# Optimization experiments

Measured on AMD Instinct MI355X. Metric: run time of the kernel, lower is better.

## Reference

```python
import jax, jax.numpy as jnp
import numpy as np

N_NODES = 50000
D = 128
N_EDGES = 800000


def _gcn_layer(h, W, b, row, col, mask, n_nodes):
    # Linear: h @ W.T + b  (nn.Linear convention)
    h = h @ W.T + b
    # degree of source nodes, counting only non-self-loop edges (remove_self_loops)
    deg = jax.ops.segment_sum(mask.astype(h.dtype), row, num_segments=n_nodes)
    deg_inv_sqrt = jnp.where(deg > 0, jax.lax.rsqrt(jnp.maximum(deg, 1.0)), 0.0)
    norm = deg_inv_sqrt[row] * deg_inv_sqrt[col] * mask.astype(h.dtype)
    # gather-scale messages [E, D], scatter-add into target nodes (col)
    msg = norm[:, None] * h[row]
    return jax.ops.segment_sum(msg, col, num_segments=n_nodes)


def setup_inputs() -> dict:
    key = jax.random.key(0)
    ks = jax.random.split(key, 9)
    x = jax.random.normal(ks[0], (N_NODES, D), dtype=jnp.float32)
    edge_index = jax.random.randint(ks[1], (2, N_EDGES), 0, N_NODES, dtype=jnp.int64)
    lim = 1.0 / np.sqrt(D)
    params = {}
    for i in range(3):
        params[f"W{i}"] = jax.random.uniform(ks[2 + 2 * i], (D, D), jnp.float32, -lim, lim)
        params[f"b{i}"] = jax.random.uniform(ks[3 + 2 * i], (D,), jnp.float32, -lim, lim)
    return {"x": x, "edge_index": edge_index, **params}


def reference(x, edge_index, W0, b0, W1, b1, W2, b2):
    row, col = edge_index[0], edge_index[1]
    mask = row != col  # remove_self_loops
    h = x
    for W, b in ((W0, b0), (W1, b1), (W2, b2)):
        h_new = jax.nn.relu(_gcn_layer(h, W, b, row, col, mask, x.shape[0]))
        h = h + h_new
    return h
```

## Files before the change

### kernel.cpp

```cpp
#include <hip/hip_runtime.h>
#include <hip/hip_bf16.h>


#define D_DIM 128
#define SCAN_CHUNK 1024
#define CHUNKS 256
#define GROUPS 8
#define GS (CHUNKS / GROUPS)
#define LDSW 12512

typedef __attribute__((ext_vector_type(8))) short bf16x8;
typedef __attribute__((ext_vector_type(4))) float f32x4;

static __device__ __forceinline__ short f2bf(float f) {
    union { __hip_bfloat16 b; short s; } u;
    u.b = __float2bfloat16(f);
    return u.s;
}
static __device__ __forceinline__ float bf_lo(unsigned p) { return __uint_as_float(p << 16); }
static __device__ __forceinline__ float bf_hi(unsigned p) { return __uint_as_float(p & 0xffff0000u); }


__global__ __launch_bounds__(256) void hist_kernel(const int* __restrict__ ei,
                                                   unsigned* __restrict__ partial_col,
                                                   unsigned* __restrict__ partial_row,
                                                   int E, int CHSZ) {
    __shared__ unsigned hh[LDSW];
    int tid = threadIdx.x;
    int ch = blockIdx.x;
    int docol = (blockIdx.y == 0);
    for (int i = tid; i < LDSW; i += 256) hh[i] = 0u;
    __syncthreads();
    int e0 = ch * CHSZ, e1 = min(e0 + CHSZ, E);
    for (int e = e0 + tid; e < e1; e += 256) {
        int row = ei[e];
        int col = ei[E + e];
        if (row == col) continue;
        int bin = docol ? col : row;
        atomicAdd(&hh[bin >> 2], 1u << ((bin & 3) * 8));
    }
    __syncthreads();
    unsigned* dst = (docol ? partial_col : partial_row) + (size_t)ch * LDSW;
    for (int i = tid; i < LDSW; i += 256) dst[i] = hh[i];
}

__global__ __launch_bounds__(256) void group_prefix_kernel(
    unsigned* __restrict__ partial_col, const unsigned* __restrict__ partial_row,
    unsigned* __restrict__ gsum_col, unsigned* __restrict__ gsum_row, int NW) {
    int w = blockIdx.x * 256 + threadIdx.x;
    if (w >= NW) return;
    int g = blockIdx.y;
    size_t base = (size_t)(g * GS) * LDSW + w;
    if (blockIdx.z == 0) {
        unsigned run = 0;
#pragma unroll 4
        for (int c = 0; c < GS; c++) {
            unsigned v = partial_col[base + (size_t)c * LDSW];
            partial_col[base + (size_t)c * LDSW] = run;
            run += v;
        }
        gsum_col[g * NW + w] = run;
    } else {
        unsigned run = 0;
#pragma unroll 4
        for (int c = 0; c < GS; c++) run += partial_row[base + (size_t)c * LDSW];
        gsum_row[g * NW + w] = run;
    }
}

__global__ __launch_bounds__(256) void cnt_dis_kernel(
    const unsigned* __restrict__ gsum_col, const unsigned* __restrict__ gsum_row,
    int* __restrict__ col_cnt, float* __restrict__ dis, int* __restrict__ bsum, int NW) {
    __shared__ int wsum[4];
    int w = blockIdx.x * 256 + threadIdx.x;
    int s = 0;
    if (w < NW) {
        unsigned clo = 0, chi = 0, rlo = 0, rhi = 0;
#pragma unroll
        for (int g = 0; g < GROUPS; g++) {
            unsigned wc = gsum_col[g * NW + w];
            unsigned wr = gsum_row[g * NW + w];
            clo += wc & 0x00FF00FFu; chi += (wc >> 8) & 0x00FF00FFu;
            rlo += wr & 0x00FF00FFu; rhi += (wr >> 8) & 0x00FF00FFu;
        }
        int c0 = clo & 0xFFFF, c1 = chi & 0xFFFF, c2 = clo >> 16, c3 = chi >> 16;
        int r0 = rlo & 0xFFFF, r1 = rhi & 0xFFFF, r2 = rlo >> 16, r3 = rhi >> 16;
        ((int4*)col_cnt)[w] = make_int4(c0, c1, c2, c3);
        float4 dv;
        dv.x = (r0 > 0) ? rsqrtf((float)r0) : 0.0f;
        dv.y = (r1 > 0) ? rsqrtf((float)r1) : 0.0f;
        dv.z = (r2 > 0) ? rsqrtf((float)r2) : 0.0f;
        dv.w = (r3 > 0) ? rsqrtf((float)r3) : 0.0f;
        ((float4*)dis)[w] = dv;
        s = c0 + c1 + c2 + c3;
    }
#pragma unroll
    for (int d = 32; d > 0; d >>= 1) s += __shfl_down(s, d, 64);
    int lane = threadIdx.x & 63, wv = threadIdx.x >> 6;
    if (lane == 0) wsum[wv] = s;
    __syncthreads();
    if (threadIdx.x == 0) bsum[blockIdx.x] = wsum[0] + wsum[1] + wsum[2] + wsum[3];
}

__global__ __launch_bounds__(64) void scan_bbase_kernel(const int* __restrict__ bsum,
                                                        int* __restrict__ bbase,
                                                        int* __restrict__ offs,
                                                        int G, int n) {
    int lane = threadIdx.x;
    int v = (lane < G) ? bsum[lane] : 0;
    int s = v;
#pragma unroll
    for (int d = 1; d < 64; d <<= 1) {
        int t = __shfl_up(s, d, 64);
        if (lane >= d) s += t;
    }
    if (lane < G) bbase[lane] = s - v;
    if (lane == 63) offs[n] = s;
}

__global__ __launch_bounds__(256) void scan_final_kernel(const int* __restrict__ cnt,
                                                         const int* __restrict__ bbase,
                                                         int* __restrict__ offs, int n) {
    __shared__ int wsum[4];
    int base = blockIdx.x * SCAN_CHUNK;
    int tid = threadIdx.x;
    const int PT = SCAN_CHUNK / 256;
    int v[PT];
    int s = 0;
#pragma unroll
    for (int i = 0; i < PT; i++) {
        int g = base + tid * PT + i;
        v[i] = (g < n) ? cnt[g] : 0;
        s += v[i];
    }
    int local_sum = s;
    int lane = tid & 63, w = tid >> 6;
#pragma unroll
    for (int d = 1; d < 64; d <<= 1) {
        int t = __shfl_up(s, d, 64);
        if (lane >= d) s += t;
    }
    if (lane == 63) wsum[w] = s;
    __syncthreads();
    int wbase = 0;
    for (int i = 0; i < w; i++) wbase += wsum[i];
    int run = bbase[blockIdx.x] + wbase + (s - local_sum);
#pragma unroll
    for (int i = 0; i < PT; i++) {
        int g = base + tid * PT + i;
        if (g < n) offs[g] = run;
        run += v[i];
    }
}

__global__ __launch_bounds__(256) void group_base_kernel(
    unsigned* __restrict__ partial_col, const unsigned* __restrict__ gsum_col, int NW) {
    int w = blockIdx.x * 256 + threadIdx.x;
    if (w >= NW) return;
    int g = blockIdx.y + 1;
    unsigned gb = 0;
    for (int gp = 0; gp < g; gp++) gb += gsum_col[gp * NW + w];
    size_t base = (size_t)(g * GS) * LDSW + w;
#pragma unroll 4
    for (int c = 0; c < GS; c++) partial_col[base + (size_t)c * LDSW] += gb;
}

__global__ __launch_bounds__(256) void scatter_kernel(const int* __restrict__ ei,
                                                      const float* __restrict__ dis,
                                                      const int* __restrict__ offs,
                                                      const unsigned* __restrict__ chpref,
                                                      unsigned* __restrict__ epack,
                                                      int E, int CHSZ) {
    __shared__ unsigned cur[LDSW];
    int tid = threadIdx.x;
    int ch = blockIdx.x;
    for (int i = tid; i < LDSW; i += 256) cur[i] = 0u;
    __syncthreads();
    int e0 = ch * CHSZ, e1 = min(e0 + CHSZ, E);
    const unsigned* pf = chpref + (size_t)ch * LDSW;
    for (int e = e0 + tid; e < e1; e += 256) {
        int row = ei[e];
        int col = ei[E + e];
        if (row == col) continue;
        float wgt = dis[row] * dis[col];
        int wd = col >> 2, sh = (col & 3) * 8;
        unsigned old = atomicAdd(&cur[wd], 1u << sh);
        int slot = offs[col] + (int)((pf[wd] >> sh) & 0xFFu) + (int)((old >> sh) & 0xFFu);
        epack[slot] = (unsigned)row | ((unsigned)(unsigned short)f2bf(wgt) << 16);
    }
}

__global__ void wcvt_all_kernel(const float* __restrict__ W0, const float* __restrict__ W1,
                                const float* __restrict__ W2, unsigned short* __restrict__ B0,
                                unsigned short* __restrict__ B1, unsigned short* __restrict__ B2) {
    int i = blockIdx.x * blockDim.x + threadIdx.x;
    const float* W = (blockIdx.y == 0) ? W0 : (blockIdx.y == 1) ? W1 : W2;
    unsigned short* B = (blockIdx.y == 0) ? B0 : (blockIdx.y == 1) ? B1 : B2;
    if (i < D_DIM * D_DIM) B[i] = (unsigned short)f2bf(W[i]);
}


__global__ __launch_bounds__(256) void linear_mfma_kernel(
    const float* __restrict__ A, const unsigned short* __restrict__ Wb,
    const float* __restrict__ bias, unsigned short* __restrict__ hWb, int nrows) {
    __shared__ unsigned short stage[4][16 * 136];
    int wave = threadIdx.x >> 6;
    int lane = threadIdx.x & 63;
    int r0 = blockIdx.x * 64 + wave * 16;
    int m = lane & 15, q = lane >> 4;
    int rload = min(r0 + m, nrows - 1);
    const float4* h4 = (const float4*)A;

    f32x4 acc[8];
#pragma unroll
    for (int jt = 0; jt < 8; jt++) acc[jt] = (f32x4){0.f, 0.f, 0.f, 0.f};

#pragma unroll
    for (int k0 = 0; k0 < 128; k0 += 32) {
        int c0 = k0 + q * 8;
        float4 x0 = h4[rload * 32 + (c0 >> 2)];
        float4 x1 = h4[rload * 32 + (c0 >> 2) + 1];
        bf16x8 a;
        a[0] = f2bf(x0.x); a[1] = f2bf(x0.y); a[2] = f2bf(x0.z); a[3] = f2bf(x0.w);
        a[4] = f2bf(x1.x); a[5] = f2bf(x1.y); a[6] = f2bf(x1.z); a[7] = f2bf(x1.w);
#pragma unroll
        for (int jt = 0; jt < 8; jt++) {
            bf16x8 b = *(const bf16x8*)(Wb + (jt * 16 + m) * D_DIM + c0);
            acc[jt] = __builtin_amdgcn_mfma_f32_16x16x32_bf16(a, b, acc[jt], 0, 0, 0);
        }
    }

#pragma unroll
    for (int jt = 0; jt < 8; jt++) {
        float bv = bias[jt * 16 + m];
#pragma unroll
        for (int reg = 0; reg < 4; reg++)
            stage[wave][(q * 4 + reg) * 136 + jt * 16 + m] =
                (unsigned short)f2bf(acc[jt][reg] + bv);
    }
#pragma unroll
    for (int t = 0; t < 4; t++) {
        int rl = t * 4 + (lane >> 4);
        int gr = r0 + rl;
        if (gr < nrows) {
            uint4 v = *(const uint4*)&stage[wave][rl * 136 + (lane & 15) * 8];
            *(uint4*)&hWb[(size_t)gr * D_DIM + (lane & 15) * 8] = v;
        }
    }
}

__global__ __launch_bounds__(256) void agg_kernel(const int* __restrict__ offs,
                                                  const unsigned* __restrict__ epack,
                                                  const unsigned int* __restrict__ hW2,
                                                  const float* __restrict__ hprev,
                                                  float* __restrict__ hout, int n_nodes) {
    int node = (int)((blockIdx.x * blockDim.x + threadIdx.x) >> 6);
    int lane = threadIdx.x & 63;
    if (node >= n_nodes) return;

    int beg = offs[node];
    int end = offs[node + 1];

    float ax8[8], ay8[8];
#pragma unroll
    for (int u = 0; u < 8; u++) { ax8[u] = 0.f; ay8[u] = 0.f; }

    int i = beg;
    for (; i + 8 <= end; i += 8) {
        unsigned e[8];
        unsigned p[8];
#pragma unroll
        for (int u = 0; u < 8; u++) e[u] = epack[i + u];
#pragma unroll
        for (int u = 0; u < 8; u++) p[u] = hW2[((e[u] & 0xffffu) << 6) + lane];
#pragma unroll
        for (int u = 0; u < 8; u++) {
            float w = bf_hi(e[u]);
            ax8[u] = fmaf(w, bf_lo(p[u]), ax8[u]);
            ay8[u] = fmaf(w, bf_hi(p[u]), ay8[u]);
        }
    }
    int rem = end - i;
    if (rem & 4) {
        unsigned e[4];
        unsigned p[4];
#pragma unroll
        for (int u = 0; u < 4; u++) e[u] = epack[i + u];
#pragma unroll
        for (int u = 0; u < 4; u++) p[u] = hW2[((e[u] & 0xffffu) << 6) + lane];
#pragma unroll
        for (int u = 0; u < 4; u++) {
            float w = bf_hi(e[u]);
            ax8[u] = fmaf(w, bf_lo(p[u]), ax8[u]);
            ay8[u] = fmaf(w, bf_hi(p[u]), ay8[u]);
        }
        i += 4;
    }
    if (rem & 2) {
        unsigned e0 = epack[i], e1 = epack[i + 1];
        unsigned p0 = hW2[((e0 & 0xffffu) << 6) + lane];
        unsigned p1 = hW2[((e1 & 0xffffu) << 6) + lane];
        float w0 = bf_hi(e0), w1 = bf_hi(e1);
        ax8[4] = fmaf(w0, bf_lo(p0), ax8[4]); ay8[4] = fmaf(w0, bf_hi(p0), ay8[4]);
        ax8[5] = fmaf(w1, bf_lo(p1), ax8[5]); ay8[5] = fmaf(w1, bf_hi(p1), ay8[5]);
        i += 2;
    }
    if (rem & 1) {
        unsigned e0 = epack[i];
        unsigned p0 = hW2[((e0 & 0xffffu) << 6) + lane];
        float w0 = bf_hi(e0);
        ax8[6] = fmaf(w0, bf_lo(p0), ax8[6]); ay8[6] = fmaf(w0, bf_hi(p0), ay8[6]);
    }
    float ax = ((ax8[0] + ax8[1]) + (ax8[2] + ax8[3])) + ((ax8[4] + ax8[5]) + (ax8[6] + ax8[7]));
    float ay = ((ay8[0] + ay8[1]) + (ay8[2] + ay8[3])) + ((ay8[4] + ay8[5]) + (ay8[6] + ay8[7]));

    int idx = node * (D_DIM / 2) + lane;
    float2 hv = ((const float2*)hprev)[idx];
    float2 o;
    o.x = hv.x + fmaxf(ax, 0.0f);
    o.y = hv.y + fmaxf(ay, 0.0f);
    ((float2*)hout)[idx] = o;
}


static inline size_t align_up(size_t x, size_t a) { return (x + a - 1) & ~(a - 1); }

extern "C" void kernel_launch(void* const* d_in, const int* in_sizes, int n_in,
                              void* d_out, int out_size, void* d_ws, size_t ws_size,
                              hipStream_t stream) {
    const float* x = (const float*)d_in[0];
    const int* ei = (const int*)d_in[1];
    const float* Wl[3] = {(const float*)d_in[2], (const float*)d_in[4], (const float*)d_in[6]};
    const float* bl[3] = {(const float*)d_in[3], (const float*)d_in[5], (const float*)d_in[7]};

    const int N = in_sizes[0] / D_DIM;
    const int E = in_sizes[1] / 2;
    const int NW = N / 4;
    const int G = (N + SCAN_CHUNK - 1) / SCAN_CHUNK;
    const int NWB = (NW + 255) / 256;
    const int CHSZ = (E + CHUNKS - 1) / CHUNKS;

    char* p = (char*)d_ws;
    int* col_cnt = (int*)p;            p += align_up((size_t)N * 4, 256);
    int* offs    = (int*)p;            p += align_up((size_t)(N + 1) * 4, 256);
    float* dis   = (float*)p;          p += align_up((size_t)N * 4, 256);
    int* bsum    = (int*)p;            p += align_up((size_t)64 * 4, 256);
    int* bbase   = (int*)p;            p += align_up((size_t)64 * 4, 256);
    unsigned* partial_col = (unsigned*)p;  p += align_up((size_t)CHUNKS * LDSW * 4, 256);
    unsigned* partial_row = (unsigned*)p;  p += align_up((size_t)CHUNKS * LDSW * 4, 256);
    unsigned* gsum_col = (unsigned*)p; p += align_up((size_t)GROUPS * NW * 4, 256);
    unsigned* gsum_row = (unsigned*)p; p += align_up((size_t)GROUPS * NW * 4, 256);
    unsigned short* Wb[3];
    for (int l = 0; l < 3; l++) { Wb[l] = (unsigned short*)p; p += align_up((size_t)D_DIM * D_DIM * 2, 256); }
    unsigned* epack = (unsigned*)p;    p += align_up((size_t)E * 4, 256);
    unsigned short* hWb = (unsigned short*)p;  p += align_up((size_t)N * D_DIM * 2, 256);
    (void)ws_size;

    hist_kernel<<<dim3(CHUNKS, 2), 256, 0, stream>>>(ei, partial_col, partial_row, E, CHSZ);
    group_prefix_kernel<<<dim3(NWB, GROUPS, 2), 256, 0, stream>>>(partial_col, partial_row,
                                                                  gsum_col, gsum_row, NW);
    cnt_dis_kernel<<<NWB, 256, 0, stream>>>(gsum_col, gsum_row, col_cnt, dis, bsum, NW);
    scan_bbase_kernel<<<1, 64, 0, stream>>>(bsum, bbase, offs, G, N);
    scan_final_kernel<<<G, 256, 0, stream>>>(col_cnt, bbase, offs, N);
    group_base_kernel<<<dim3(NWB, GROUPS - 1), 256, 0, stream>>>(partial_col, gsum_col, NW);
    scatter_kernel<<<CHUNKS, 256, 0, stream>>>(ei, dis, offs, partial_col, epack, E, CHSZ);
    wcvt_all_kernel<<<dim3((D_DIM * D_DIM + 255) / 256, 3), 256, 0, stream>>>(
        Wl[0], Wl[1], Wl[2], Wb[0], Wb[1], Wb[2]);

    const float* hprev = x;
    float* h = (float*)d_out;
    int gemm_blocks = (N + 63) / 64;
    int agg_blocks = (N + 3) / 4;
    for (int l = 0; l < 3; l++) {
        linear_mfma_kernel<<<gemm_blocks, 256, 0, stream>>>(hprev, Wb[l], bl[l], hWb, N);
        agg_kernel<<<agg_blocks, 256, 0, stream>>>(offs, epack, (const unsigned int*)hWb, hprev, h, N);
        hprev = h;
    }
}
```

Measured before the change: 316.7 us.

## Fold small preprocessing kernels into neighbors to cut launch count

The weight bf16 conversion moves into an extra blockIdx.y slice of the histogram kernel. The block-sum scan is recomputed redundantly inside each scan_final block, and the per-group base addition to partial_col is folded into scatter's LDS seeding. This removes three kernel launches and a read-modify-write pass over partial_col. In exchange, scan_final and scatter each do some redundant work per block.

```diff
diff --git a/kernel.cpp b/kernel.cpp
--- a/kernel.cpp
+++ b/kernel.cpp
@@ -24,9 +24,21 @@
 __global__ __launch_bounds__(256) void hist_kernel(const int* __restrict__ ei,
                                                    unsigned* __restrict__ partial_col,
                                                    unsigned* __restrict__ partial_row,
+                                                   const float* __restrict__ W0,
+                                                   const float* __restrict__ W1,
+                                                   const float* __restrict__ W2,
+                                                   unsigned short* __restrict__ Wb,
                                                    int E, int CHSZ) {
+    int tid = threadIdx.x;
+    if (blockIdx.y == 2) {
+        int i = blockIdx.x * 256 + tid;
+        if (i < 3 * D_DIM * D_DIM) {
+            const float* W = (i < 16384) ? W0 : (i < 32768) ? W1 : W2;
+            Wb[i] = (unsigned short)f2bf(W[i & 16383]);
+        }
+        return;
+    }
     __shared__ unsigned hh[LDSW];
-    int tid = threadIdx.x;
     int ch = blockIdx.x;
     int docol = (blockIdx.y == 0);
     for (int i = tid; i < LDSW; i += 256) hh[i] = 0u;
@@ -102,26 +114,12 @@
     if (threadIdx.x == 0) bsum[blockIdx.x] = wsum[0] + wsum[1] + wsum[2] + wsum[3];
 }
 
-__global__ __launch_bounds__(64) void scan_bbase_kernel(const int* __restrict__ bsum,
-                                                        int* __restrict__ bbase,
-                                                        int* __restrict__ offs,
-                                                        int G, int n) {
-    int lane = threadIdx.x;
-    int v = (lane < G) ? bsum[lane] : 0;
-    int s = v;
-#pragma unroll
-    for (int d = 1; d < 64; d <<= 1) {
-        int t = __shfl_up(s, d, 64);
-        if (lane >= d) s += t;
-    }
-    if (lane < G) bbase[lane] = s - v;
-    if (lane == 63) offs[n] = s;
-}
-
 __global__ __launch_bounds__(256) void scan_final_kernel(const int* __restrict__ cnt,
-                                                         const int* __restrict__ bbase,
-                                                         int* __restrict__ offs, int n) {
+                                                         const int* __restrict__ bsum,
+                                                         int* __restrict__ offs,
+                                                         int n, int G) {
     __shared__ int wsum[4];
+    __shared__ int sblock;
     int base = blockIdx.x * SCAN_CHUNK;
     int tid = threadIdx.x;
     const int PT = SCAN_CHUNK / 256;
@@ -141,10 +139,21 @@
         if (lane >= d) s += t;
     }
     if (lane == 63) wsum[w] = s;
+    if (tid < 64) {
+        int bv = (tid < G) ? bsum[tid] : 0;
+        int bs = bv;
+#pragma unroll
+        for (int d = 1; d < 64; d <<= 1) {
+            int t = __shfl_up(bs, d, 64);
+            if (tid >= d) bs += t;
+        }
+        if (tid == blockIdx.x) sblock = bs - bv;
+        if (tid == 63 && blockIdx.x == G - 1) offs[n] = bs;
+    }
     __syncthreads();
     int wbase = 0;
     for (int i = 0; i < w; i++) wbase += wsum[i];
-    int run = bbase[blockIdx.x] + wbase + (s - local_sum);
+    int run = sblock + wbase + (s - local_sum);
 #pragma unroll
     for (int i = 0; i < PT; i++) {
         int g = base + tid * PT + i;
@@ -153,31 +162,26 @@
     }
 }
 
-__global__ __launch_bounds__(256) void group_base_kernel(
-    unsigned* __restrict__ partial_col, const unsigned* __restrict__ gsum_col, int NW) {
-    int w = blockIdx.x * 256 + threadIdx.x;
-    if (w >= NW) return;
-    int g = blockIdx.y + 1;
-    unsigned gb = 0;
-    for (int gp = 0; gp < g; gp++) gb += gsum_col[gp * NW + w];
-    size_t base = (size_t)(g * GS) * LDSW + w;
-#pragma unroll 4
-    for (int c = 0; c < GS; c++) partial_col[base + (size_t)c * LDSW] += gb;
-}
-
 __global__ __launch_bounds__(256) void scatter_kernel(const int* __restrict__ ei,
                                                       const float* __restrict__ dis,
                                                       const int* __restrict__ offs,
                                                       const unsigned* __restrict__ chpref,
+                                                      const unsigned* __restrict__ gsum_col,
                                                       unsigned* __restrict__ epack,
-                                                      int E, int CHSZ) {
+                                                      int E, int CHSZ, int NW) {
     __shared__ unsigned cur[LDSW];
     int tid = threadIdx.x;
     int ch = blockIdx.x;
-    for (int i = tid; i < LDSW; i += 256) cur[i] = 0u;
+    int g = ch / GS;
+    const unsigned* pf = chpref + (size_t)ch * LDSW;
+    for (int i = tid; i < LDSW; i += 256) {
+        unsigned seed = pf[i];
+        if (i < NW)
+            for (int gp = 0; gp < g; gp++) seed += gsum_col[gp * NW + i];
+        cur[i] = seed;
+    }
     __syncthreads();
     int e0 = ch * CHSZ, e1 = min(e0 + CHSZ, E);
-    const unsigned* pf = chpref + (size_t)ch * LDSW;
     for (int e = e0 + tid; e < e1; e += 256) {
         int row = ei[e];
         int col = ei[E + e];
@@ -185,18 +189,9 @@
         float wgt = dis[row] * dis[col];
         int wd = col >> 2, sh = (col & 3) * 8;
         unsigned old = atomicAdd(&cur[wd], 1u << sh);
-        int slot = offs[col] + (int)((pf[wd] >> sh) & 0xFFu) + (int)((old >> sh) & 0xFFu);
+        int slot = offs[col] + (int)((old >> sh) & 0xFFu);
         epack[slot] = (unsigned)row | ((unsigned)(unsigned short)f2bf(wgt) << 16);
     }
-}
-
-__global__ void wcvt_all_kernel(const float* __restrict__ W0, const float* __restrict__ W1,
-                                const float* __restrict__ W2, unsigned short* __restrict__ B0,
-                                unsigned short* __restrict__ B1, unsigned short* __restrict__ B2) {
-    int i = blockIdx.x * blockDim.x + threadIdx.x;
-    const float* W = (blockIdx.y == 0) ? W0 : (blockIdx.y == 1) ? W1 : W2;
-    unsigned short* B = (blockIdx.y == 0) ? B0 : (blockIdx.y == 1) ? B1 : B2;
-    if (i < D_DIM * D_DIM) B[i] = (unsigned short)f2bf(W[i]);
 }
 
 
@@ -345,34 +340,30 @@
     int* offs    = (int*)p;            p += align_up((size_t)(N + 1) * 4, 256);
     float* dis   = (float*)p;          p += align_up((size_t)N * 4, 256);
     int* bsum    = (int*)p;            p += align_up((size_t)64 * 4, 256);
-    int* bbase   = (int*)p;            p += align_up((size_t)64 * 4, 256);
     unsigned* partial_col = (unsigned*)p;  p += align_up((size_t)CHUNKS * LDSW * 4, 256);
     unsigned* partial_row = (unsigned*)p;  p += align_up((size_t)CHUNKS * LDSW * 4, 256);
     unsigned* gsum_col = (unsigned*)p; p += align_up((size_t)GROUPS * NW * 4, 256);
     unsigned* gsum_row = (unsigned*)p; p += align_up((size_t)GROUPS * NW * 4, 256);
-    unsigned short* Wb[3];
-    for (int l = 0; l < 3; l++) { Wb[l] = (unsigned short*)p; p += align_up((size_t)D_DIM * D_DIM * 2, 256); }
+    unsigned short* Wb = (unsigned short*)p;  p += align_up((size_t)3 * D_DIM * D_DIM * 2, 256);
     unsigned* epack = (unsigned*)p;    p += align_up((size_t)E * 4, 256);
     unsigned short* hWb = (unsigned short*)p;  p += align_up((size_t)N * D_DIM * 2, 256);
     (void)ws_size;
 
-    hist_kernel<<<dim3(CHUNKS, 2), 256, 0, stream>>>(ei, partial_col, partial_row, E, CHSZ);
+    hist_kernel<<<dim3(CHUNKS, 3), 256, 0, stream>>>(ei, partial_col, partial_row,
+                                                     Wl[0], Wl[1], Wl[2], Wb, E, CHSZ);
     group_prefix_kernel<<<dim3(NWB, GROUPS, 2), 256, 0, stream>>>(partial_col, partial_row,
                                                                   gsum_col, gsum_row, NW);
     cnt_dis_kernel<<<NWB, 256, 0, stream>>>(gsum_col, gsum_row, col_cnt, dis, bsum, NW);
-    scan_bbase_kernel<<<1, 64, 0, stream>>>(bsum, bbase, offs, G, N);
-    scan_final_kernel<<<G, 256, 0, stream>>>(col_cnt, bbase, offs, N);
-    group_base_kernel<<<dim3(NWB, GROUPS - 1), 256, 0, stream>>>(partial_col, gsum_col, NW);
-    scatter_kernel<<<CHUNKS, 256, 0, stream>>>(ei, dis, offs, partial_col, epack, E, CHSZ);
-    wcvt_all_kernel<<<dim3((D_DIM * D_DIM + 255) / 256, 3), 256, 0, stream>>>(
-        Wl[0], Wl[1], Wl[2], Wb[0], Wb[1], Wb[2]);
+    scan_final_kernel<<<G, 256, 0, stream>>>(col_cnt, bsum, offs, N, G);
+    scatter_kernel<<<CHUNKS, 256, 0, stream>>>(ei, dis, offs, partial_col, gsum_col,
+                                               epack, E, CHSZ, NW);
 
     const float* hprev = x;
     float* h = (float*)d_out;
     int gemm_blocks = (N + 63) / 64;
     int agg_blocks = (N + 3) / 4;
     for (int l = 0; l < 3; l++) {
-        linear_mfma_kernel<<<gemm_blocks, 256, 0, stream>>>(hprev, Wb[l], bl[l], hWb, N);
+        linear_mfma_kernel<<<gemm_blocks, 256, 0, stream>>>(hprev, Wb + l * 16384, bl[l], hWb, N);
         agg_kernel<<<agg_blocks, 256, 0, stream>>>(offs, epack, (const unsigned int*)hWb, hprev, h, N);
         hprev = h;
     }
```

Measured after the change: 341.2 us. 7.7% more time.
